# Kernel optimization log

Measured on AMD Instinct MI355X. Metric: run time of the kernel, lower is better.

Reference implementation:

```python
import jax, jax.numpy as jnp
import numpy as np

N = 100000      # nodes
E = 1600000     # edges (avg degree 16)
EL = 200000     # supervision (label) edges
D_IN, D_HID, D_OUT = 128, 128, 64


def setup_inputs() -> dict:
    key = jax.random.key(0)
    k = jax.random.split(key, 6)
    x = jax.random.normal(k[0], (N, D_IN), jnp.float32)
    edge_index = jax.random.randint(k[1], (2, E), 0, N, dtype=jnp.int32)
    edge_label_index = jax.random.randint(k[2], (2, EL), 0, N, dtype=jnp.int32)
    W1 = jax.random.normal(k[3], (D_IN, D_HID), jnp.float32) * (1.0 / np.sqrt(D_IN))
    b1 = jnp.zeros((D_HID,), jnp.float32)
    W2 = jax.random.normal(k[4], (D_HID, D_OUT), jnp.float32) * (1.0 / np.sqrt(D_HID))
    b2 = jnp.zeros((D_OUT,), jnp.float32)
    return {"x": x, "edge_index": edge_index, "edge_label_index": edge_label_index,
            "W1": W1, "b1": b1, "W2": W2, "b2": b2}


def gcn_layer(x, src, dst, W, b, n):
    """PyG-style GCNConv: linear -> sym-normalized scatter-add with self loops -> +bias."""
    h = x @ W                                   # [N, F]
    ones = jnp.ones(src.shape[0], h.dtype)
    deg = jax.ops.segment_sum(ones, dst, num_segments=n) + 1.0   # in-degree + self loop
    dinv = jax.lax.rsqrt(deg)                   # deg^{-1/2}
    norm = dinv[src] * dinv[dst]                # per-edge norm
    agg = jax.ops.segment_sum(h[src] * norm[:, None], dst, num_segments=n)
    agg = agg + h * (1.0 / deg)[:, None]        # self-loop contribution: dinv[i]^2
    return agg + b


def reference(x, edge_index, edge_label_index, W1, b1, W2, b2):
    src, dst = edge_index[0], edge_index[1]
    z = gcn_layer(x, src, dst, W1, b1, N)
    z = jax.nn.relu(z)                          # dropout omitted (eval mode)
    z = gcn_layer(z, src, dst, W2, b2, N)
    # decode: gather-dot over supervision edges
    return (z[edge_label_index[0]] * z[edge_label_index[1]]).sum(axis=-1)
```

## Files before the change

### kernel.cpp

```cpp
#include <hip/hip_runtime.h>
#include <stdint.h>

typedef __bf16 bf16x8 __attribute__((ext_vector_type(8)));
typedef float  floatx4 __attribute__((ext_vector_type(4)));
typedef float  floatx2 __attribute__((ext_vector_type(2)));
typedef __fp16 h2 __attribute__((ext_vector_type(2)));

__device__ __forceinline__ unsigned short f2b(float x){
    unsigned u = __float_as_uint(x);
    u = u + 0x7FFFu + ((u >> 16) & 1u);
    return (unsigned short)(u >> 16);
}
__device__ __forceinline__ float b2f(unsigned short h){
    return __uint_as_float(((unsigned)h) << 16);
}
__device__ __forceinline__ unsigned char f2f8(float x){
    int p = __builtin_amdgcn_cvt_pk_fp8_f32(x, x, 0, false);
    return (unsigned char)(p & 0xff);
}

__global__ __launch_bounds__(256) void k_scatter2(const int* __restrict__ src,
                                                  const int* __restrict__ dst,
                                                  int* __restrict__ gcur,
                                                  unsigned* __restrict__ slab,
                                                  int E_, int nbins){
    __shared__ int h[1024];
    __shared__ unsigned wbuf[4096];
    __shared__ unsigned short bbuf[4096];
    int t = threadIdx.x, blk = blockIdx.x;
    for (int i = t; i < nbins; i += 256) h[i] = 0;
    __syncthreads();
    int base = blk * 4096;
    int valid = E_ - base; if (valid > 4096) valid = 4096;
    #pragma unroll
    for (int j = 0; j < 4; j++){
        int li = (j * 256 + t) * 4;
        int e = base + li;
        if (e < E_){
            int4 d = *(const int4*)(dst + e);
            int4 s = *(const int4*)(src + e);
            wbuf[li + 0] = ((unsigned)(d.x & 127) << 25) | (unsigned)s.x;
            wbuf[li + 1] = ((unsigned)(d.y & 127) << 25) | (unsigned)s.y;
            wbuf[li + 2] = ((unsigned)(d.z & 127) << 25) | (unsigned)s.z;
            wbuf[li + 3] = ((unsigned)(d.w & 127) << 25) | (unsigned)s.w;
            bbuf[li + 0] = (unsigned short)(d.x >> 7);
            bbuf[li + 1] = (unsigned short)(d.y >> 7);
            bbuf[li + 2] = (unsigned short)(d.z >> 7);
            bbuf[li + 3] = (unsigned short)(d.w >> 7);
            atomicAdd(&h[d.x >> 7], 1);
            atomicAdd(&h[d.y >> 7], 1);
            atomicAdd(&h[d.z >> 7], 1);
            atomicAdd(&h[d.w >> 7], 1);
        }
    }
    __syncthreads();
    for (int i = t; i < nbins; i += 256){
        int hv = h[i];
        h[i] = hv ? atomicAdd(&gcur[i], hv) : 0;
    }
    __syncthreads();
    for (int i = t; i < valid; i += 256){
        int bin = bbuf[i];
        int p = atomicAdd(&h[bin], 1);
        slab[(size_t)bin * 4096 + p] = wbuf[i];
    }
}

__global__ __launch_bounds__(256) void k_binsort(const unsigned* __restrict__ slab,
                                                 const int* __restrict__ gcur,
                                                 int* __restrict__ csr,
                                                 int* __restrict__ cnt,
                                                 int* __restrict__ off,
                                                 float* __restrict__ dinv,
                                                 int n, int nbins){
    int b = blockIdx.x, t = threadIdx.x;
    __shared__ int sv[1024], sp[256];
    #pragma unroll
    for (int k = 0; k < 4; k++){
        int i = t * 4 + k;
        sv[i] = (i < nbins) ? gcur[i] : 0;
    }
    __syncthreads();
    int a0 = sv[t * 4], a1 = sv[t * 4 + 1], a2 = sv[t * 4 + 2], a3 = sv[t * 4 + 3];
    sp[t] = a0 + a1 + a2 + a3;
    __syncthreads();
    for (int o = 1; o < 256; o <<= 1){
        int v = (t >= o) ? sp[t - o] : 0;
        __syncthreads();
        sp[t] += v;
        __syncthreads();
    }
    int basep = t ? sp[t - 1] : 0;
    sv[t * 4]     = basep;
    sv[t * 4 + 1] = basep + a0;
    sv[t * 4 + 2] = basep + a0 + a1;
    sv[t * 4 + 3] = basep + a0 + a1 + a2;
    __syncthreads();
    int s0 = sv[b];
    int len = gcur[b];
    if (len > 4096) len = 4096;
    const unsigned* seg = slab + (size_t)b * 4096;
    __shared__ int cl[128], sc[128], cur[128];
    __shared__ unsigned buf[4096], outb[4096];
    if (t < 128){ cl[t] = 0; cur[t] = 0; }
    __syncthreads();
    for (int i = t; i < len; i += 256) buf[i] = seg[i];
    __syncthreads();
    for (int i = t; i < len; i += 256) atomicAdd(&cl[buf[i] >> 25], 1);
    __syncthreads();
    if (t < 128) sc[t] = cl[t];
    __syncthreads();
    for (int o = 1; o < 128; o <<= 1){
        int v = 0;
        if (t < 128 && t >= o) v = sc[t - o];
        __syncthreads();
        if (t < 128) sc[t] += v;
        __syncthreads();
    }
    for (int i = t; i < len; i += 256){
        unsigned w = buf[i];
        int nd = (int)(w >> 25);
        int p = (sc[nd] - cl[nd]) + atomicAdd(&cur[nd], 1);
        outb[p] = w & 0x1FFFFFFu;
    }
    __syncthreads();
    for (int i = t; i < len; i += 256) csr[s0 + i] = (int)outb[i];
    if (t < 128){
        int node = b * 128 + t;
        if (node < n){
            cnt[node] = cl[t];
            off[node] = s0 + (sc[t] - cl[t]);
            dinv[node] = rsqrtf((float)cl[t] + 1.0f);
        }
    }
}

__global__ __launch_bounds__(256) void k_init(const float* __restrict__ W1,
                                              const float* __restrict__ W2,
                                              unsigned short* __restrict__ wf1,
                                              unsigned* __restrict__ w2p,
                                              int* __restrict__ gcur, int nbins){
    int blk = blockIdx.x, t = threadIdx.x;
    if (blk == 24){
        for (int i = t; i < nbins; i += 256) gcur[i] = 0;
        return;
    }
    int f = blk * 256 + t;
    if (f < 2048){
        int lane = f & 63;
        int ctkc = f >> 6;
        int kc = ctkc & 3, ct = ctkc >> 2;
        int col = ct * 16 + (lane & 15);
        int k0  = kc * 32 + (lane >> 4) * 8;
        unsigned short* d = wf1 + (size_t)f * 8;
        #pragma unroll
        for (int j = 0; j < 8; j++) d[j] = f2b(W1[(k0 + j) * 128 + col]);
    } else if (f < 2048 + 4096){
        int lf = f - 2048;
        int kp = lf >> 6, lane = lf & 63;
        h2 p = __builtin_amdgcn_cvt_pkrtz(W2[(2 * kp) * 64 + lane],
                                          W2[(2 * kp + 1) * 64 + lane]);
        w2p[lf] = __builtin_bit_cast(unsigned, p);
    }
}

__global__ __launch_bounds__(256) void k_gemm1(const float* __restrict__ x,
                                               const unsigned short* __restrict__ wf,
                                               const float* __restrict__ dinv,
                                               unsigned char* __restrict__ hs, int n){
    __shared__ unsigned short Wl[16384];
    __shared__ unsigned short Al[64 * 136];
    int t = threadIdx.x;
    long rowBase = (long)blockIdx.x * 64;
    {
        const uint4* s4 = (const uint4*)wf;
        uint4* d4 = (uint4*)Wl;
        #pragma unroll
        for (int i = 0; i < 8; i++) d4[t + i * 256] = s4[t + i * 256];
    }
    {
        const float4* xs = (const float4*)(x + rowBase * 128);
        #pragma unroll
        for (int k = 0; k < 8; k++){
            int i = t + k * 256;
            int r = i >> 5, c4 = (i & 31) << 2;
            float4 v = make_float4(0.f, 0.f, 0.f, 0.f);
            if (rowBase + r < n) v = xs[i];
            unsigned lo = (unsigned)f2b(v.x) | ((unsigned)f2b(v.y) << 16);
            unsigned hi = (unsigned)f2b(v.z) | ((unsigned)f2b(v.w) << 16);
            *(uint2*)&Al[r * 136 + c4] = make_uint2(lo, hi);
        }
    }
    __syncthreads();
    int w = t >> 6, lane = t & 63, lr = lane & 15, q = lane >> 4;
    floatx4 zero = {0.f, 0.f, 0.f, 0.f};
    floatx4 acc[8];
    #pragma unroll
    for (int ct = 0; ct < 8; ct++) acc[ct] = zero;
    #pragma unroll
    for (int kc = 0; kc < 4; kc++){
        bf16x8 af = *(const bf16x8*)&Al[(w * 16 + lr) * 136 + kc * 32 + q * 8];
        #pragma unroll
        for (int ct = 0; ct < 8; ct++){
            bf16x8 bf = *(const bf16x8*)&Wl[((ct * 4 + kc) * 64 + lane) * 8];
            acc[ct] = __builtin_amdgcn_mfma_f32_16x16x32_bf16(af, bf, acc[ct], 0, 0, 0);
        }
    }
    long r0 = rowBase + w * 16 + q * 4;
    #pragma unroll
    for (int r = 0; r < 4; r++){
        long row = r0 + r;
        if (row >= n) continue;
        float dv = dinv[row];
        unsigned char* orow = hs + row * 128 + lr;
        #pragma unroll
        for (int ct = 0; ct < 8; ct++) orow[ct * 16] = f2f8(acc[ct][r] * dv);
    }
}

__global__ __launch_bounds__(256) void k_agg1g2(const unsigned char* __restrict__ hs,
                                                const int* __restrict__ off,
                                                const int* __restrict__ cnt,
                                                const int* __restrict__ csr,
                                                const float* __restrict__ dinv,
                                                const float* __restrict__ b1,
                                                const unsigned* __restrict__ w2p,
                                                unsigned short* __restrict__ hs2,
                                                int n, int nwaves){
    __shared__ unsigned W2l[4096];
    __shared__ unsigned zp[4][64];
    int t = threadIdx.x;
    {
        const uint4* w4 = (const uint4*)w2p;
        uint4* d4 = (uint4*)W2l;
        #pragma unroll
        for (int i = 0; i < 4; i++) d4[t + i * 256] = w4[t + i * 256];
    }
    __syncthreads();
    int wband = t >> 6, lane = t & 63;
    float2 bb = ((const float2*)b1)[lane];
    for (int wid = blockIdx.x * 4 + wband; wid < n; wid += nwaves){
        size_t i = (size_t)wid;
        int start = off[wid], c = cnt[wid];
        unsigned short v0 = *(const unsigned short*)(hs + i * 128 + lane * 2);
        floatx2 f0 = __builtin_amdgcn_cvt_pk_f32_fp8((int)v0, false);
        float a0 = f0.x, a1 = f0.y;
        int j = 0;
        for (; j + 8 <= c; j += 8){
            size_t s0 = (size_t)csr[start + j + 0];
            size_t s1 = (size_t)csr[start + j + 1];
            size_t s2 = (size_t)csr[start + j + 2];
            size_t s3 = (size_t)csr[start + j + 3];
            size_t s4 = (size_t)csr[start + j + 4];
            size_t s5 = (size_t)csr[start + j + 5];
            size_t s6 = (size_t)csr[start + j + 6];
            size_t s7 = (size_t)csr[start + j + 7];
            unsigned short w0 = *(const unsigned short*)(hs + s0 * 128 + lane * 2);
            unsigned short w1 = *(const unsigned short*)(hs + s1 * 128 + lane * 2);
            unsigned short w2 = *(const unsigned short*)(hs + s2 * 128 + lane * 2);
            unsigned short w3 = *(const unsigned short*)(hs + s3 * 128 + lane * 2);
            unsigned short w4 = *(const unsigned short*)(hs + s4 * 128 + lane * 2);
            unsigned short w5 = *(const unsigned short*)(hs + s5 * 128 + lane * 2);
            unsigned short w6 = *(const unsigned short*)(hs + s6 * 128 + lane * 2);
            unsigned short w7 = *(const unsigned short*)(hs + s7 * 128 + lane * 2);
            floatx2 g0 = __builtin_amdgcn_cvt_pk_f32_fp8((int)w0, false);
            floatx2 g1 = __builtin_amdgcn_cvt_pk_f32_fp8((int)w1, false);
            floatx2 g2 = __builtin_amdgcn_cvt_pk_f32_fp8((int)w2, false);
            floatx2 g3 = __builtin_amdgcn_cvt_pk_f32_fp8((int)w3, false);
            floatx2 g4 = __builtin_amdgcn_cvt_pk_f32_fp8((int)w4, false);
            floatx2 g5 = __builtin_amdgcn_cvt_pk_f32_fp8((int)w5, false);
            floatx2 g6 = __builtin_amdgcn_cvt_pk_f32_fp8((int)w6, false);
            floatx2 g7 = __builtin_amdgcn_cvt_pk_f32_fp8((int)w7, false);
            a0 += g0.x; a1 += g0.y;
            a0 += g1.x; a1 += g1.y;
            a0 += g2.x; a1 += g2.y;
            a0 += g3.x; a1 += g3.y;
            a0 += g4.x; a1 += g4.y;
            a0 += g5.x; a1 += g5.y;
            a0 += g6.x; a1 += g6.y;
            a0 += g7.x; a1 += g7.y;
        }
        for (; j < c; j++){
            size_t s = (size_t)csr[start + j];
            unsigned short v = *(const unsigned short*)(hs + s * 128 + lane * 2);
            floatx2 g = __builtin_amdgcn_cvt_pk_f32_fp8((int)v, false);
            a0 += g.x; a1 += g.y;
        }
        float dv = dinv[wid];
        float z0 = fmaxf(fmaf(dv, a0, bb.x), 0.f);
        float z1 = fmaxf(fmaf(dv, a1, bb.y), 0.f);
        zp[wband][lane] = __builtin_bit_cast(unsigned, __builtin_amdgcn_cvt_pkrtz(z0, z1));
        float acc0 = 0.f, acc1 = 0.f;
        #pragma unroll 8
        for (int kp = 0; kp < 64; kp += 2){
            h2 wa = __builtin_bit_cast(h2, W2l[kp * 64 + lane]);
            h2 wb = __builtin_bit_cast(h2, W2l[(kp + 1) * 64 + lane]);
            h2 za = __builtin_bit_cast(h2, zp[wband][kp]);
            h2 zb = __builtin_bit_cast(h2, zp[wband][kp + 1]);
            acc0 = __builtin_amdgcn_fdot2(za, wa, acc0, false);
            acc1 = __builtin_amdgcn_fdot2(zb, wb, acc1, false);
        }
        hs2[i * 64 + lane] = f2b((acc0 + acc1) * dv);
    }
}

__global__ __launch_bounds__(256) void k_agg2(const unsigned short* __restrict__ hs,
                                              const int* __restrict__ off,
                                              const int* __restrict__ cnt,
                                              const int* __restrict__ csr,
                                              const float* __restrict__ dinv,
                                              const float* __restrict__ b,
                                              unsigned short* __restrict__ z, int n){
    int wv = (blockIdx.x * 256 + threadIdx.x) >> 6;
    int lane = threadIdx.x & 63;
    int half = lane >> 5, hl = lane & 31;
    int node = wv * 2 + half;
    if (node >= n) return;
    size_t i = (size_t)node;
    int start = off[node], c = cnt[node];
    unsigned v0 = *(const unsigned*)(hs + i * 64 + hl * 2);
    float a0 = b2f((unsigned short)v0);
    float a1 = b2f((unsigned short)(v0 >> 16));
    int j = 0;
    for (; j + 8 <= c; j += 8){
        size_t s0 = (size_t)csr[start + j + 0];
        size_t s1 = (size_t)csr[start + j + 1];
        size_t s2 = (size_t)csr[start + j + 2];
        size_t s3 = (size_t)csr[start + j + 3];
        size_t s4 = (size_t)csr[start + j + 4];
        size_t s5 = (size_t)csr[start + j + 5];
        size_t s6 = (size_t)csr[start + j + 6];
        size_t s7 = (size_t)csr[start + j + 7];
        unsigned w0 = *(const unsigned*)(hs + s0 * 64 + hl * 2);
        unsigned w1 = *(const unsigned*)(hs + s1 * 64 + hl * 2);
        unsigned w2 = *(const unsigned*)(hs + s2 * 64 + hl * 2);
        unsigned w3 = *(const unsigned*)(hs + s3 * 64 + hl * 2);
        unsigned w4 = *(const unsigned*)(hs + s4 * 64 + hl * 2);
        unsigned w5 = *(const unsigned*)(hs + s5 * 64 + hl * 2);
        unsigned w6 = *(const unsigned*)(hs + s6 * 64 + hl * 2);
        unsigned w7 = *(const unsigned*)(hs + s7 * 64 + hl * 2);
        a0 += b2f((unsigned short)w0); a1 += b2f((unsigned short)(w0 >> 16));
        a0 += b2f((unsigned short)w1); a1 += b2f((unsigned short)(w1 >> 16));
        a0 += b2f((unsigned short)w2); a1 += b2f((unsigned short)(w2 >> 16));
        a0 += b2f((unsigned short)w3); a1 += b2f((unsigned short)(w3 >> 16));
        a0 += b2f((unsigned short)w4); a1 += b2f((unsigned short)(w4 >> 16));
        a0 += b2f((unsigned short)w5); a1 += b2f((unsigned short)(w5 >> 16));
        a0 += b2f((unsigned short)w6); a1 += b2f((unsigned short)(w6 >> 16));
        a0 += b2f((unsigned short)w7); a1 += b2f((unsigned short)(w7 >> 16));
    }
    for (; j < c; j++){
        size_t s = (size_t)csr[start + j];
        unsigned v = *(const unsigned*)(hs + s * 64 + hl * 2);
        a0 += b2f((unsigned short)v);
        a1 += b2f((unsigned short)(v >> 16));
    }
    float dv = dinv[node];
    float2 bb = ((const float2*)b)[hl];
    float r0 = fmaf(dv, a0, bb.x);
    float r1 = fmaf(dv, a1, bb.y);
    *(unsigned*)(z + i * 64 + hl * 2) = (unsigned)f2b(r0) | ((unsigned)f2b(r1) << 16);
}

__global__ __launch_bounds__(256) void k_decode(const unsigned short* __restrict__ z,
                                                const int* __restrict__ es,
                                                const int* __restrict__ et,
                                                float* __restrict__ out, int m){
    int wv = (blockIdx.x * 256 + threadIdx.x) >> 6;
    int lane = threadIdx.x & 63;
    int e = wv * 4 + (lane >> 4);
    int ql = lane & 15;
    float p = 0.f;
    if (e < m){
        size_t s = (size_t)es[e], t2 = (size_t)et[e];
        uint2 vs = *(const uint2*)(z + s * 64 + ql * 4);
        uint2 vt = *(const uint2*)(z + t2 * 64 + ql * 4);
        p = b2f((unsigned short)vs.x) * b2f((unsigned short)vt.x)
          + b2f((unsigned short)(vs.x >> 16)) * b2f((unsigned short)(vt.x >> 16))
          + b2f((unsigned short)vs.y) * b2f((unsigned short)vt.y)
          + b2f((unsigned short)(vs.y >> 16)) * b2f((unsigned short)(vt.y >> 16));
    }
    #pragma unroll
    for (int o = 8; o > 0; o >>= 1) p += __shfl_xor(p, o);
    if (ql == 0 && e < m) out[e] = p;
}


extern "C" void kernel_launch(void* const* d_in, const int* in_sizes, int n_in,
                              void* d_out, int out_size, void* d_ws, size_t ws_size,
                              hipStream_t stream){
    const float* x   = (const float*)d_in[0];
    const int*   ei  = (const int*)d_in[1];
    const int*   eli = (const int*)d_in[2];
    const float* W1  = (const float*)d_in[3];
    const float* b1  = (const float*)d_in[4];
    const float* W2  = (const float*)d_in[5];
    const float* b2  = (const float*)d_in[6];
    float* out = (float*)d_out;

    int N_  = in_sizes[0] / 128;
    int E_  = in_sizes[1] / 2;
    int EL_ = in_sizes[2] / 2;
    int NBINS = (N_ + 127) >> 7;
    const int EPB = 4096;
    int NBLK = (E_ + EPB - 1) / EPB;

    char* w = (char*)d_ws;
    size_t o = 0;
    auto alloc = [&](size_t bytes) -> size_t {
        size_t r = o; o += (bytes + 511) & ~(size_t)511; return r;
    };
    size_t o_cnt  = alloc((size_t)N_ * 4);
    size_t o_off  = alloc((size_t)N_ * 4);
    size_t o_dinv = alloc((size_t)N_ * 4);
    size_t o_gcur = alloc((size_t)NBINS * 4);
    size_t o_csr  = alloc((size_t)E_ * 4);
    size_t o_wf1  = alloc(16384 * 2);
    size_t o_w2p  = alloc(4096 * 4);
    size_t o_slab = alloc((size_t)NBINS * 4096 * 4);
    size_t o_hs1  = alloc((size_t)N_ * 128);
    size_t o_hs2  = alloc((size_t)N_ * 64 * 2);

    int* cnt  = (int*)(w + o_cnt);
    int* off  = (int*)(w + o_off);
    float* dinv = (float*)(w + o_dinv);
    int* gcur = (int*)(w + o_gcur);
    int* csr  = (int*)(w + o_csr);
    unsigned short* wf1 = (unsigned short*)(w + o_wf1);
    unsigned* w2p = (unsigned*)(w + o_w2p);
    unsigned* slab = (unsigned*)(w + o_slab);
    unsigned char* hs1 = (unsigned char*)(w + o_hs1);
    unsigned short* hs2 = (unsigned short*)(w + o_hs2);
    unsigned short* z2  = (unsigned short*)(w + o_slab);

    const int AGG1_BLOCKS = 2048;
    int nwaves = AGG1_BLOCKS * 4;

    k_init    <<<25, 256, 0, stream>>>(W1, W2, wf1, w2p, gcur, NBINS);
    k_scatter2<<<NBLK, 256, 0, stream>>>(ei, ei + E_, gcur, slab, E_, NBINS);
    k_binsort <<<NBINS, 256, 0, stream>>>(slab, gcur, csr, cnt, off, dinv, N_, NBINS);
    k_gemm1   <<<(N_ + 63) / 64, 256, 0, stream>>>(x, wf1, dinv, hs1, N_);
    k_agg1g2  <<<AGG1_BLOCKS, 256, 0, stream>>>(hs1, off, cnt, csr, dinv, b1, w2p, hs2, N_, nwaves);
    k_agg2    <<<(N_ + 7) / 8, 256, 0, stream>>>(hs2, off, cnt, csr, dinv, b2, z2, N_);
    k_decode  <<<(EL_ + 15) / 16, 256, 0, stream>>>(z2, eli, eli + EL_, out, EL_);
}
```

Before: 271.4 us.

## Slice layer-2 features into 8-column tables and aggregate per slice for cache locality

The layer-2 pre-aggregation features are now written as eight column-slice tables (each 8 bf16 per node) instead of row-major 64-wide rows. The aggregation kernel assigns each block a slice, so the gathered table it touches is one eighth the size and more likely to stay in L2 cache, and it processes 8 nodes per wave with a grid-stride loop. In exchange every CSR index list is read eight times, each gather moves only 16 bytes, and the output writes are scattered across slices.

After: 300.8 us. 10.8% more time.

```diff
diff --git a/kernel.cpp b/kernel.cpp
--- a/kernel.cpp
+++ b/kernel.cpp
@@ -300,7 +300,7 @@
             acc0 = __builtin_amdgcn_fdot2(za, wa, acc0, false);
             acc1 = __builtin_amdgcn_fdot2(zb, wb, acc1, false);
         }
-        hs2[i * 64 + lane] = f2b((acc0 + acc1) * dv);
+        hs2[((size_t)(lane >> 3) * n + i) * 8 + (lane & 7)] = f2b((acc0 + acc1) * dv);
     }
 }
 
@@ -309,56 +309,43 @@
                                               const int* __restrict__ cnt,
                                               const int* __restrict__ csr,
                                               const float* __restrict__ dinv,
-                                              const float* __restrict__ b,
-                                              unsigned short* __restrict__ z, int n){
-    int wv = (blockIdx.x * 256 + threadIdx.x) >> 6;
-    int lane = threadIdx.x & 63;
-    int half = lane >> 5, hl = lane & 31;
-    int node = wv * 2 + half;
-    if (node >= n) return;
-    size_t i = (size_t)node;
-    int start = off[node], c = cnt[node];
-    unsigned v0 = *(const unsigned*)(hs + i * 64 + hl * 2);
-    float a0 = b2f((unsigned short)v0);
-    float a1 = b2f((unsigned short)(v0 >> 16));
-    int j = 0;
-    for (; j + 8 <= c; j += 8){
-        size_t s0 = (size_t)csr[start + j + 0];
-        size_t s1 = (size_t)csr[start + j + 1];
-        size_t s2 = (size_t)csr[start + j + 2];
-        size_t s3 = (size_t)csr[start + j + 3];
-        size_t s4 = (size_t)csr[start + j + 4];
-        size_t s5 = (size_t)csr[start + j + 5];
-        size_t s6 = (size_t)csr[start + j + 6];
-        size_t s7 = (size_t)csr[start + j + 7];
-        unsigned w0 = *(const unsigned*)(hs + s0 * 64 + hl * 2);
-        unsigned w1 = *(const unsigned*)(hs + s1 * 64 + hl * 2);
-        unsigned w2 = *(const unsigned*)(hs + s2 * 64 + hl * 2);
-        unsigned w3 = *(const unsigned*)(hs + s3 * 64 + hl * 2);
-        unsigned w4 = *(const unsigned*)(hs + s4 * 64 + hl * 2);
-        unsigned w5 = *(const unsigned*)(hs + s5 * 64 + hl * 2);
-        unsigned w6 = *(const unsigned*)(hs + s6 * 64 + hl * 2);
-        unsigned w7 = *(const unsigned*)(hs + s7 * 64 + hl * 2);
-        a0 += b2f((unsigned short)w0); a1 += b2f((unsigned short)(w0 >> 16));
-        a0 += b2f((unsigned short)w1); a1 += b2f((unsigned short)(w1 >> 16));
-        a0 += b2f((unsigned short)w2); a1 += b2f((unsigned short)(w2 >> 16));
-        a0 += b2f((unsigned short)w3); a1 += b2f((unsigned short)(w3 >> 16));
-        a0 += b2f((unsigned short)w4); a1 += b2f((unsigned short)(w4 >> 16));
-        a0 += b2f((unsigned short)w5); a1 += b2f((unsigned short)(w5 >> 16));
-        a0 += b2f((unsigned short)w6); a1 += b2f((unsigned short)(w6 >> 16));
-        a0 += b2f((unsigned short)w7); a1 += b2f((unsigned short)(w7 >> 16));
-    }
-    for (; j < c; j++){
-        size_t s = (size_t)csr[start + j];
-        unsigned v = *(const unsigned*)(hs + s * 64 + hl * 2);
-        a0 += b2f((unsigned short)v);
-        a1 += b2f((unsigned short)(v >> 16));
-    }
-    float dv = dinv[node];
-    float2 bb = ((const float2*)b)[hl];
-    float r0 = fmaf(dv, a0, bb.x);
-    float r1 = fmaf(dv, a1, bb.y);
-    *(unsigned*)(z + i * 64 + hl * 2) = (unsigned)f2b(r0) | ((unsigned)f2b(r1) << 16);
+                                              const float* __restrict__ b2,
+                                              unsigned short* __restrict__ z2,
+                                              int n, int wps){
+    int t = threadIdx.x;
+    int slice = blockIdx.x & 7;
+    int wband = t >> 6, lane = t & 63;
+    int g = lane >> 3, h = lane & 7;
+    const unsigned short* tab = hs + (size_t)slice * n * 8;
+    float bb = b2[slice * 8 + h];
+    int wIdx = (blockIdx.x >> 3) * 4 + wband;
+    int nchunks = (n + 7) >> 3;
+    for (int cw = wIdx; cw < nchunks; cw += wps){
+        int wid = cw * 8 + g;
+        if (wid < n){
+            int start = off[wid];
+            int c = cnt[wid];
+            float dv = dinv[wid];
+            float a = b2f(tab[(size_t)wid * 8 + h]);
+            int j = 0;
+            for (; j + 4 <= c; j += 4){
+                int s0 = csr[start + j];
+                int s1 = csr[start + j + 1];
+                int s2 = csr[start + j + 2];
+                int s3 = csr[start + j + 3];
+                unsigned short w0 = tab[(size_t)s0 * 8 + h];
+                unsigned short w1 = tab[(size_t)s1 * 8 + h];
+                unsigned short w2 = tab[(size_t)s2 * 8 + h];
+                unsigned short w3 = tab[(size_t)s3 * 8 + h];
+                a += b2f(w0); a += b2f(w1); a += b2f(w2); a += b2f(w3);
+            }
+            for (; j < c; j++){
+                int s = csr[start + j];
+                a += b2f(tab[(size_t)s * 8 + h]);
+            }
+            z2[(size_t)wid * 64 + slice * 8 + h] = f2b(fmaf(dv, a, bb));
+        }
+    }
 }
 
 __global__ __launch_bounds__(256) void k_decode(const unsigned short* __restrict__ z,
@@ -434,12 +421,14 @@
 
     const int AGG1_BLOCKS = 2048;
     int nwaves = AGG1_BLOCKS * 4;
+    const int AGG2_BLOCKS = 2048;
+    int wps = (AGG2_BLOCKS / 8) * 4;
 
     k_init    <<<25, 256, 0, stream>>>(W1, W2, wf1, w2p, gcur, NBINS);
     k_scatter2<<<NBLK, 256, 0, stream>>>(ei, ei + E_, gcur, slab, E_, NBINS);
     k_binsort <<<NBINS, 256, 0, stream>>>(slab, gcur, csr, cnt, off, dinv, N_, NBINS);
     k_gemm1   <<<(N_ + 63) / 64, 256, 0, stream>>>(x, wf1, dinv, hs1, N_);
     k_agg1g2  <<<AGG1_BLOCKS, 256, 0, stream>>>(hs1, off, cnt, csr, dinv, b1, w2p, hs2, N_, nwaves);
-    k_agg2    <<<(N_ + 7) / 8, 256, 0, stream>>>(hs2, off, cnt, csr, dinv, b2, z2, N_);
+    k_agg2    <<<AGG2_BLOCKS, 256, 0, stream>>>(hs2, off, cnt, csr, dinv, b2, z2, N_, wps);
     k_decode  <<<(EL_ + 15) / 16, 256, 0, stream>>>(z2, eli, eli + EL_, out, EL_);
 }
```
